# Optimization experiments

Measured on AMD Instinct MI355X. Metric: run time of the kernel, lower is better.

## Reference

```python
import jax, jax.numpy as jnp
import numpy as np

# dims
M, C, D = 64, 2000, 512          # clients, classes, embed_dim
H = 4                             # num_heads
HD = D // H                       # head_dim = 128
DFF = 2048                        # torch TransformerEncoderLayer default dim_feedforward
NUM_CLASSES = 2000
EPS = 1e-5


def _ln(x, g, b):
    mu = jnp.mean(x, axis=-1, keepdims=True)
    var = jnp.mean(jnp.square(x - mu), axis=-1, keepdims=True)
    return (x - mu) * jax.lax.rsqrt(var + EPS) * g + b


def setup_inputs() -> dict:
    key = jax.random.key(0)
    ks = jax.random.split(key, 16)
    s = 0.02
    return {
        "client_protos": jax.random.normal(ks[0], (M, C, D), jnp.float32),
        "norm_g": jnp.ones((D,), jnp.float32),
        "norm_b": jnp.zeros((D,), jnp.float32),
        "in_proj_w": jax.random.normal(ks[1], (3 * D, D), jnp.float32) * s,
        "in_proj_b": jnp.zeros((3 * D,), jnp.float32),
        "out_proj_w": jax.random.normal(ks[2], (D, D), jnp.float32) * s,
        "out_proj_b": jnp.zeros((D,), jnp.float32),
        "lin1_w": jax.random.normal(ks[3], (DFF, D), jnp.float32) * s,
        "lin1_b": jnp.zeros((DFF,), jnp.float32),
        "lin2_w": jax.random.normal(ks[4], (D, DFF), jnp.float32) * s,
        "lin2_b": jnp.zeros((D,), jnp.float32),
        "norm1_g": jnp.ones((D,), jnp.float32),
        "norm1_b": jnp.zeros((D,), jnp.float32),
        "norm2_g": jnp.ones((D,), jnp.float32),
        "norm2_b": jnp.zeros((D,), jnp.float32),
        "global_query": jax.random.normal(ks[5], (NUM_CLASSES, D), jnp.float32),
        "all_labels": jax.random.randint(ks[6], (C,), 0, NUM_CLASSES, jnp.int32),
        "round_num": 10,
        "client_idx": 0,
    }


def reference(client_protos, norm_g, norm_b, in_proj_w, in_proj_b,
              out_proj_w, out_proj_b, lin1_w, lin1_b, lin2_w, lin2_b,
              norm1_g, norm1_b, norm2_g, norm2_b, global_query,
              all_labels, round_num, client_idx):
    # 1) LayerNorm over all prototypes: (M, C, D)
    x = _ln(client_protos, norm_g, norm_b)
    # 2) Per-class transformer: original loops c in range(C) on (1, M, D).
    #    Batched: treat C as batch -> (C, M, D). Post-norm torch encoder layer.
    x = jnp.transpose(x, (1, 0, 2))  # (C, M, D)
    # self-attention
    qkv = x @ in_proj_w.T + in_proj_b          # (C, M, 3D)
    q, k, v = jnp.split(qkv, 3, axis=-1)
    q = q.reshape(C, M, H, HD)
    k = k.reshape(C, M, H, HD)
    v = v.reshape(C, M, H, HD)
    scores = jnp.einsum('cqhd,ckhd->chqk', q, k) / np.sqrt(HD).astype(np.float32)
    attn = jax.nn.softmax(scores, axis=-1)
    sa = jnp.einsum('chqk,ckhd->cqhd', attn, v).reshape(C, M, D)
    sa = sa @ out_proj_w.T + out_proj_b
    x = _ln(x + sa, norm1_g, norm1_b)
    # feed-forward (relu, dropout = eval no-op)
    ff = jax.nn.relu(x @ lin1_w.T + lin1_b) @ lin2_w.T + lin2_b
    x = _ln(x + ff, norm2_g, norm2_b)           # (C, M, D) == protos_trans^T
    # 3) Cross-attention with per-class global query
    q_all = global_query[all_labels].reshape(C, H, HD)
    kv_all = x.reshape(C, M, H, HD)
    s2 = jnp.einsum('chd,cmhd->chm', q_all, kv_all) / np.sqrt(HD).astype(np.float32)
    w2 = jax.nn.softmax(s2, axis=-1)
    attn_out = jnp.einsum('chm,cmhd->chd', w2, kv_all).reshape(C, D)
    return attn_out
```

## Files before the change

### kernel.cpp

```cpp
#include <hip/hip_runtime.h>

typedef _Float16 f16;
typedef _Float16 half4 __attribute__((ext_vector_type(4)));
typedef _Float16 half8 __attribute__((ext_vector_type(8)));
typedef float f32x4 __attribute__((ext_vector_type(4)));

typedef __attribute__((address_space(1))) void* as1v;
typedef __attribute__((address_space(3))) void* as3v;

#define SCALE 0.08838834764831845f

static __device__ __forceinline__ f32x4 mfma16(half8 a, half8 b, f32x4 c){
  return __builtin_amdgcn_mfma_f32_16x16x32_f16(a, b, c, 0, 0, 0);
}

__global__ __launch_bounds__(256) void k_cvt(const float* __restrict__ src, f16* __restrict__ dst, int n){
  int i = (blockIdx.x * 256 + threadIdx.x) * 8;
  if (i >= n) return;
  float4 a = *(const float4*)(src + i);
  float4 b = *(const float4*)(src + i + 4);
  half8 h;
  h[0] = (f16)a.x; h[1] = (f16)a.y; h[2] = (f16)a.z; h[3] = (f16)a.w;
  h[4] = (f16)b.x; h[5] = (f16)b.y; h[6] = (f16)b.z; h[7] = (f16)b.w;
  *(half8*)(dst + i) = h;
}

__global__ __launch_bounds__(256) void k_ln0(const float* __restrict__ protos,
                                             const float* __restrict__ g,
                                             const float* __restrict__ bb,
                                             f16* __restrict__ xb, int c0){
  const int w = threadIdx.x >> 6, l = threadIdx.x & 63;
  const int q = blockIdx.x * 4 + w;
  const int cl = q >> 6, m = q & 63;
  const float* in = protos + ((size_t)m * 2000 + (size_t)(c0 + cl)) * 512;
  const int d0 = l * 8;
  float4 a = *(const float4*)(in + d0);
  float4 c = *(const float4*)(in + d0 + 4);
  float s  = a.x + a.y + a.z + a.w + c.x + c.y + c.z + c.w;
  float ss = a.x*a.x + a.y*a.y + a.z*a.z + a.w*a.w + c.x*c.x + c.y*c.y + c.z*c.z + c.w*c.w;
#pragma unroll
  for (int msk = 1; msk < 64; msk <<= 1){ s += __shfl_xor(s, msk); ss += __shfl_xor(ss, msk); }
  const float mu = s * (1.f/512.f);
  const float rs = rsqrtf(ss * (1.f/512.f) - mu*mu + 1e-5f);
  float4 g0 = *(const float4*)(g + d0),  g1 = *(const float4*)(g + d0 + 4);
  float4 b0 = *(const float4*)(bb + d0), b1 = *(const float4*)(bb + d0 + 4);
  half8 o;
  o[0] = (f16)((a.x - mu) * rs * g0.x + b0.x);
  o[1] = (f16)((a.y - mu) * rs * g0.y + b0.y);
  o[2] = (f16)((a.z - mu) * rs * g0.z + b0.z);
  o[3] = (f16)((a.w - mu) * rs * g0.w + b0.w);
  o[4] = (f16)((c.x - mu) * rs * g1.x + b1.x);
  o[5] = (f16)((c.y - mu) * rs * g1.y + b1.y);
  o[6] = (f16)((c.z - mu) * rs * g1.z + b1.z);
  o[7] = (f16)((c.w - mu) * rs * g1.w + b1.w);
  *(half8*)(xb + (size_t)q * 512 + d0) = o;
}

__global__ __launch_bounds__(256) void k_resln(const f16* __restrict__ t, const f16* __restrict__ skip,
                                               const float* __restrict__ g, const float* __restrict__ bb,
                                               f16* __restrict__ outp){
  const int w = threadIdx.x >> 6, l = threadIdx.x & 63;
  const size_t q = (size_t)blockIdx.x * 4 + w;
  const int d0 = l * 8;
  half8 tv = *(const half8*)(t + q * 512 + d0);
  half8 sk = *(const half8*)(skip + q * 512 + d0);
  float v0 = (float)tv[0] + (float)sk[0], v1 = (float)tv[1] + (float)sk[1];
  float v2 = (float)tv[2] + (float)sk[2], v3 = (float)tv[3] + (float)sk[3];
  float v4 = (float)tv[4] + (float)sk[4], v5 = (float)tv[5] + (float)sk[5];
  float v6 = (float)tv[6] + (float)sk[6], v7 = (float)tv[7] + (float)sk[7];
  float s  = v0+v1+v2+v3+v4+v5+v6+v7;
  float ss = v0*v0+v1*v1+v2*v2+v3*v3+v4*v4+v5*v5+v6*v6+v7*v7;
#pragma unroll
  for (int msk = 1; msk < 64; msk <<= 1){ s += __shfl_xor(s, msk); ss += __shfl_xor(ss, msk); }
  const float mu = s * (1.f/512.f);
  const float rs = rsqrtf(ss * (1.f/512.f) - mu*mu + 1e-5f);
  float4 g0 = *(const float4*)(g + d0),  g1 = *(const float4*)(g + d0 + 4);
  float4 b0 = *(const float4*)(bb + d0), b1 = *(const float4*)(bb + d0 + 4);
  half8 o;
  o[0] = (f16)((v0 - mu) * rs * g0.x + b0.x);
  o[1] = (f16)((v1 - mu) * rs * g0.y + b0.y);
  o[2] = (f16)((v2 - mu) * rs * g0.z + b0.z);
  o[3] = (f16)((v3 - mu) * rs * g0.w + b0.w);
  o[4] = (f16)((v4 - mu) * rs * g1.x + b1.x);
  o[5] = (f16)((v5 - mu) * rs * g1.y + b1.y);
  o[6] = (f16)((v6 - mu) * rs * g1.z + b1.z);
  o[7] = (f16)((v7 - mu) * rs * g1.w + b1.w);
  *(half8*)(outp + q * 512 + d0) = o;
}

#define GLL(gp, lp) __builtin_amdgcn_global_load_lds((as1v)(void*)(gp), (as3v)(lp), 16, 0, 0)

template<bool RELU>
__global__ __launch_bounds__(512, 2) void k_gemm(const f16* __restrict__ A, const f16* __restrict__ B,
                                                 const float* __restrict__ bias, f16* __restrict__ Cout,
                                                 int N, int K, int gn){
  extern __shared__ char smem_raw[];
  f16* lds = (f16*)smem_raw;

  const int t = threadIdx.x, w = t >> 6, l = t & 63;
  const int wr = w >> 2, wc = w & 3;

  const int nwg = gridDim.x;
  const int q8 = nwg >> 3, r8 = nwg & 7;
  const int xcd = blockIdx.x & 7, lidx = blockIdx.x >> 3;
  const int swz = (xcd < r8 ? xcd * (q8 + 1) : r8 * (q8 + 1) + (xcd - r8) * q8) + lidx;
  const int tm = swz / gn, tn = swz % gn;
  const size_t row0 = (size_t)tm * 256;
  const int col0 = tn * 256;

  f32x4 acc[8][4];
#pragma unroll
  for (int m = 0; m < 8; ++m)
#pragma unroll
    for (int n = 0; n < 4; ++n) acc[m][n] = (f32x4){0.f,0.f,0.f,0.f};

  const int lsw = ((t & 7) ^ ((t >> 3) & 7)) * 8;
  const f16* gAb = A + (row0 + (size_t)(t >> 3)) * (size_t)K + lsw;
  const f16* gBb = B + ((size_t)col0 + (size_t)(t >> 3)) * (size_t)K + lsw;
  const int t8 = t * 8;

  const int rA  = (l & 15) * 64;
  const int ps0 = (((l >> 4) ^ (l & 7)) << 3);
  const int ps1 = (((4 + (l >> 4)) ^ (l & 7)) << 3);
  const int abase = wr * 8192 + rA;
  const int bbase = 16384 + wc * 4096 + rA;

  const int NT = K >> 6;

  auto stgA = [&](int tt, int h){
    f16* d = lds + (tt & 1) * 32768 + h * 8192 + t8;
    const f16* s = gAb + (size_t)(h * 128) * K + (size_t)tt * 64;
    GLL(s, d);
    GLL(s + (size_t)64 * K, d + 4096);
  };
  auto stgB = [&](int tt, int h){
    f16* d = lds + (tt & 1) * 32768 + 16384 + h * 8192 + t8;
    const f16* s = gBb + (size_t)(h * 128) * K + (size_t)tt * 64;
    GLL(s, d);
    GLL(s + (size_t)64 * K, d + 4096);
  };

  stgA(0, 0); stgA(0, 1); stgB(0, 0); stgB(0, 1);
  if (NT > 1){
    stgA(1, 0);
    asm volatile("s_waitcnt vmcnt(2)" ::: "memory");
  } else {
    asm volatile("s_waitcnt vmcnt(0)" ::: "memory");
  }
  __builtin_amdgcn_s_barrier();

  for (int tt = 0; tt < NT; ++tt){
    const f16* sb = lds + (tt & 1) * 32768;
    const bool s1 = tt + 1 < NT, s2 = tt + 2 < NT;
    half8 af03[4][2], af47[4][2], bf[4][2];

#pragma unroll
    for (int m = 0; m < 4; ++m){
      af03[m][0] = *(const half8*)(sb + abase + m * 1024 + ps0);
      af03[m][1] = *(const half8*)(sb + abase + m * 1024 + ps1);
    }
#pragma unroll
    for (int n = 0; n < 2; ++n){
      bf[n][0] = *(const half8*)(sb + bbase + n * 1024 + ps0);
      bf[n][1] = *(const half8*)(sb + bbase + n * 1024 + ps1);
    }
    if (s1) stgA(tt + 1, 1);
    __builtin_amdgcn_s_barrier();
    asm volatile("s_waitcnt lgkmcnt(0)" ::: "memory");
    __builtin_amdgcn_sched_barrier(0);
    __builtin_amdgcn_s_setprio(1);
#pragma unroll
    for (int ks = 0; ks < 2; ++ks)
#pragma unroll
      for (int m = 0; m < 4; ++m)
#pragma unroll
        for (int n = 0; n < 2; ++n)
          acc[m][n] = mfma16(bf[n][ks], af03[m][ks], acc[m][n]);
    __builtin_amdgcn_s_setprio(0);
    __builtin_amdgcn_s_barrier();

#pragma unroll
    for (int n = 2; n < 4; ++n){
      bf[n][0] = *(const half8*)(sb + bbase + n * 1024 + ps0);
      bf[n][1] = *(const half8*)(sb + bbase + n * 1024 + ps1);
    }
    if (s1) stgB(tt + 1, 0);
    __builtin_amdgcn_s_barrier();
    asm volatile("s_waitcnt lgkmcnt(0)" ::: "memory");
    __builtin_amdgcn_sched_barrier(0);
    __builtin_amdgcn_s_setprio(1);
#pragma unroll
    for (int ks = 0; ks < 2; ++ks)
#pragma unroll
      for (int m = 0; m < 4; ++m)
#pragma unroll
        for (int n = 2; n < 4; ++n)
          acc[m][n] = mfma16(bf[n][ks], af03[m][ks], acc[m][n]);
    __builtin_amdgcn_s_setprio(0);
    __builtin_amdgcn_s_barrier();

#pragma unroll
    for (int m = 0; m < 4; ++m){
      af47[m][0] = *(const half8*)(sb + abase + (m + 4) * 1024 + ps0);
      af47[m][1] = *(const half8*)(sb + abase + (m + 4) * 1024 + ps1);
    }
    if (s1) stgB(tt + 1, 1);
    __builtin_amdgcn_s_barrier();
    asm volatile("s_waitcnt lgkmcnt(0)" ::: "memory");
    __builtin_amdgcn_sched_barrier(0);
    __builtin_amdgcn_s_setprio(1);
#pragma unroll
    for (int ks = 0; ks < 2; ++ks)
#pragma unroll
      for (int m = 0; m < 4; ++m)
#pragma unroll
        for (int n = 0; n < 2; ++n)
          acc[m + 4][n] = mfma16(bf[n][ks], af47[m][ks], acc[m + 4][n]);
    __builtin_amdgcn_s_setprio(0);
    __builtin_amdgcn_s_barrier();

    if (s2) stgA(tt + 2, 0);
    __builtin_amdgcn_s_barrier();
    __builtin_amdgcn_s_setprio(1);
#pragma unroll
    for (int ks = 0; ks < 2; ++ks)
#pragma unroll
      for (int m = 0; m < 4; ++m)
#pragma unroll
        for (int n = 2; n < 4; ++n)
          acc[m + 4][n] = mfma16(bf[n][ks], af47[m][ks], acc[m + 4][n]);
    __builtin_amdgcn_s_setprio(0);
    if (s1){
      if (s2) { asm volatile("s_waitcnt vmcnt(2)" ::: "memory"); }
      else    { asm volatile("s_waitcnt vmcnt(0)" ::: "memory"); }
    }
    __builtin_amdgcn_s_barrier();
  }

#pragma unroll
  for (int n = 0; n < 4; ++n){
    const int c = col0 + wc * 64 + n * 16 + ((l >> 4) << 2);
    float4 b4 = *(const float4*)(bias + c);
#pragma unroll
    for (int m = 0; m < 8; ++m){
      const size_t r = row0 + (size_t)(wr * 128 + m * 16 + (l & 15));
      float v0 = acc[m][n][0] + b4.x;
      float v1 = acc[m][n][1] + b4.y;
      float v2 = acc[m][n][2] + b4.z;
      float v3 = acc[m][n][3] + b4.w;
      if (RELU){ v0 = fmaxf(v0, 0.f); v1 = fmaxf(v1, 0.f); v2 = fmaxf(v2, 0.f); v3 = fmaxf(v3, 0.f); }
      half4 h; h[0] = (f16)v0; h[1] = (f16)v1; h[2] = (f16)v2; h[3] = (f16)v3;
      *(half4*)&Cout[r * (size_t)N + c] = h;
    }
  }
}

__global__ __launch_bounds__(256) void k_attn(const f16* __restrict__ qkv, f16* __restrict__ sa){
  __shared__ __align__(16) f16 P[4][4096];
  __shared__ __align__(16) f16 VT[4][4096];
  const int cl = blockIdx.x;
  const int h = threadIdx.x >> 6, l = threadIdx.x & 63;
  const f16* base = qkv + (size_t)cl * 64 * 1536;
  const f16* Qp = base + h * 128;
  const f16* Kp = base + 512 + h * 128;
  const f16* Vp = base + 1024 + h * 128;

  f32x4 s[4][4];
#pragma unroll
  for (int x = 0; x < 4; ++x)
#pragma unroll
    for (int y = 0; y < 4; ++y) s[x][y] = (f32x4){0.f,0.f,0.f,0.f};
#pragma unroll
  for (int ks = 0; ks < 4; ++ks){
    half8 aq[4], bk[4];
#pragma unroll
    for (int x = 0; x < 4; ++x)
      aq[x] = *(const half8*)&Qp[(size_t)(x * 16 + (l & 15)) * 1536 + ks * 32 + (l >> 4) * 8];
#pragma unroll
    for (int y = 0; y < 4; ++y)
      bk[y] = *(const half8*)&Kp[(size_t)(y * 16 + (l & 15)) * 1536 + ks * 32 + (l >> 4) * 8];
#pragma unroll
    for (int x = 0; x < 4; ++x)
#pragma unroll
      for (int y = 0; y < 4; ++y)
        s[x][y] = mfma16(aq[x], bk[y], s[x][y]);
  }

  char* Pb = (char*)&P[h][0];
#pragma unroll
  for (int x = 0; x < 4; ++x){
#pragma unroll
    for (int j = 0; j < 4; ++j){
      float e0 = s[x][0][j] * SCALE;
      float e1 = s[x][1][j] * SCALE;
      float e2 = s[x][2][j] * SCALE;
      float e3 = s[x][3][j] * SCALE;
      float mx = fmaxf(fmaxf(e0, e1), fmaxf(e2, e3));
#pragma unroll
      for (int msk = 1; msk < 16; msk <<= 1) mx = fmaxf(mx, __shfl_xor(mx, msk));
      e0 = __expf(e0 - mx); e1 = __expf(e1 - mx); e2 = __expf(e2 - mx); e3 = __expf(e3 - mx);
      float sm = e0 + e1 + e2 + e3;
#pragma unroll
      for (int msk = 1; msk < 16; msk <<= 1) sm += __shfl_xor(sm, msk);
      const float inv = 1.f / sm;
      const int row = x * 16 + (l >> 4) * 4 + j;
      const int rb = row * 128 + (l & 15) * 2;
      const int rsw = (row & 7) << 4;
      *(f16*)(Pb + ((rb     ) ^ rsw)) = (f16)(e0 * inv);
      *(f16*)(Pb + ((rb + 32) ^ rsw)) = (f16)(e1 * inv);
      *(f16*)(Pb + ((rb + 64) ^ rsw)) = (f16)(e2 * inv);
      *(f16*)(Pb + ((rb + 96) ^ rsw)) = (f16)(e3 * inv);
    }
  }

  char* Vb = (char*)&VT[h][0];
#pragma unroll
  for (int dh = 0; dh < 2; ++dh){
#pragma unroll
    for (int it = 0; it < 8; ++it){
      const int chunk = it * 64 + l;
      const int m = chunk >> 3, dc = chunk & 7;
      half8 v = *(const half8*)&Vp[(size_t)m * 1536 + dh * 64 + dc * 8];
#pragma unroll
      for (int jj = 0; jj < 8; ++jj){
        const int dd = dc * 8 + jj;
        *(f16*)(Vb + ((dd * 128 + m * 2) ^ ((dd & 7) << 4))) = v[jj];
      }
    }
    __syncthreads();
#pragma unroll
    for (int x = 0; x < 4; ++x){
      const int ar = x * 16 + (l & 15);
      const int ab = ar * 128, sw = (ar & 7) << 4;
      half8 ap0 = *(const half8*)(Pb + ((ab + (l >> 4) * 16) ^ sw));
      half8 ap1 = *(const half8*)(Pb + ((ab + 64 + (l >> 4) * 16) ^ sw));
#pragma unroll
      for (int dt = 0; dt < 4; ++dt){
        const int vr = dt * 16 + (l & 15);
        const int vb = vr * 128, vsw = (vr & 7) << 4;
        half8 b0 = *(const half8*)(Vb + ((vb + (l >> 4) * 16) ^ vsw));
        half8 b1 = *(const half8*)(Vb + ((vb + 64 + (l >> 4) * 16) ^ vsw));
        f32x4 o = (f32x4){0.f,0.f,0.f,0.f};
        o = mfma16(ap0, b0, o);
        o = mfma16(ap1, b1, o);
#pragma unroll
        for (int j = 0; j < 4; ++j){
          const int mrow = x * 16 + (l >> 4) * 4 + j;
          const int dcol = dh * 64 + dt * 16 + (l & 15);
          sa[((size_t)cl * 64 + mrow) * 512 + h * 128 + dcol] = (f16)o[j];
        }
      }
    }
    __syncthreads();
  }
}

__global__ __launch_bounds__(256) void k_cross(const f16* __restrict__ z, const float* __restrict__ gq,
                                               const int* __restrict__ labels, float* __restrict__ out,
                                               int c0){
  const int cl = blockIdx.x;
  const int h = threadIdx.x >> 6, l = threadIdx.x & 63;
  const int cg = c0 + cl;
  const float* q = gq + (size_t)labels[cg] * 512 + h * 128;
  const f16* zb = z + (size_t)cl * 64 * 512 + h * 128;

  const f16* zr = zb + (size_t)l * 512;
  float s = 0.f;
#pragma unroll
  for (int d = 0; d < 128; d += 8){
    half8 v = *(const half8*)&zr[d];
    float4 q0 = *(const float4*)&q[d];
    float4 q1 = *(const float4*)&q[d + 4];
    s += q0.x*(float)v[0] + q0.y*(float)v[1] + q0.z*(float)v[2] + q0.w*(float)v[3]
       + q1.x*(float)v[4] + q1.y*(float)v[5] + q1.z*(float)v[6] + q1.w*(float)v[7];
  }
  s *= SCALE;
  float mx = s;
#pragma unroll
  for (int msk = 1; msk < 64; msk <<= 1) mx = fmaxf(mx, __shfl_xor(mx, msk));
  float e = __expf(s - mx);
  float sm = e;
#pragma unroll
  for (int msk = 1; msk < 64; msk <<= 1) sm += __shfl_xor(sm, msk);
  const float wgt = e / sm;

  float a0 = 0.f, a1 = 0.f;
  for (int m = 0; m < 64; ++m){
    const float wm = __shfl(wgt, m);
    const f16* zm = zb + (size_t)m * 512 + 2 * l;
    a0 += wm * (float)zm[0];
    a1 += wm * (float)zm[1];
  }
  float2 o; o.x = a0; o.y = a1;
  *(float2*)&out[(size_t)cg * 512 + h * 128 + 2 * l] = o;
}

extern "C" void kernel_launch(void* const* d_in, const int* in_sizes, int n_in,
                              void* d_out, int out_size, void* d_ws, size_t ws_size,
                              hipStream_t stream){
  (void)in_sizes; (void)n_in; (void)out_size;
  const float* protos = (const float*)d_in[0];
  const float* norm_g = (const float*)d_in[1];
  const float* norm_b = (const float*)d_in[2];
  const float* in_w   = (const float*)d_in[3];
  const float* in_b   = (const float*)d_in[4];
  const float* ow     = (const float*)d_in[5];
  const float* ob     = (const float*)d_in[6];
  const float* l1w    = (const float*)d_in[7];
  const float* l1b    = (const float*)d_in[8];
  const float* l2w    = (const float*)d_in[9];
  const float* l2b    = (const float*)d_in[10];
  const float* n1g    = (const float*)d_in[11];
  const float* n1b    = (const float*)d_in[12];
  const float* n2g    = (const float*)d_in[13];
  const float* n2b    = (const float*)d_in[14];
  const float* gq     = (const float*)d_in[15];
  const int*   labels = (const int*)d_in[16];
  float* out = (float*)d_out;

  char* p = (char*)d_ws;
  auto alloc = [&](size_t bytes)->char*{
    char* r = p; p += (bytes + 255) & ~(size_t)255; return r;
  };
  f16* Wq = (f16*)alloc((size_t)1536*512*2);
  f16* Wo = (f16*)alloc((size_t)512*512*2);
  f16* W1 = (f16*)alloc((size_t)2048*512*2);
  f16* W2 = (f16*)alloc((size_t)512*2048*2);
  const size_t fixed = (size_t)(p - (char*)d_ws);

  const size_t per_class = (size_t)64*512*2 + (size_t)64*2048*2 + (size_t)64*512*2 + (size_t)64*512*2;
  long long avail = (long long)ws_size - (long long)fixed - 8192;
  long long cc_max = avail > 0 ? avail / (long long)per_class : 0;
  int Cc = (int)(cc_max > 2000 ? 2000 : cc_max);
  Cc &= ~3;
  if (Cc < 4) Cc = 4;

  f16* xb  = (f16*)alloc((size_t)Cc*64*512*2);
  f16* big = (f16*)alloc((size_t)Cc*64*2048*2);
  f16* sac = (f16*)alloc((size_t)Cc*64*512*2);
  f16* tmp = (f16*)alloc((size_t)Cc*64*512*2);

  k_cvt<<<1536*512/2048, 256, 0, stream>>>(in_w, Wq, 1536*512);
  k_cvt<<<512*512/2048,  256, 0, stream>>>(ow,   Wo, 512*512);
  k_cvt<<<2048*512/2048, 256, 0, stream>>>(l1w,  W1, 2048*512);
  k_cvt<<<2048*512/2048, 256, 0, stream>>>(l2w,  W2, 512*2048);

  const size_t SMEM = 131072;
  for (int c0 = 0; c0 < 2000; c0 += Cc){
    const int cc = (2000 - c0 < Cc) ? (2000 - c0) : Cc;
    const int R = cc * 64;
    const int gm = R / 256;
    k_ln0<<<R/4, 256, 0, stream>>>(protos, norm_g, norm_b, xb, c0);
    k_gemm<false><<<gm*6, 512, SMEM, stream>>>(xb, Wq, in_b, big, 1536, 512, 6);
    k_attn<<<cc, 256, 0, stream>>>(big, sac);
    k_gemm<false><<<gm*2, 512, SMEM, stream>>>(sac, Wo, ob, tmp, 512, 512, 2);
    k_resln<<<R/4, 256, 0, stream>>>(tmp, xb, n1g, n1b, sac);
    k_gemm<true><<<gm*8, 512, SMEM, stream>>>(sac, W1, l1b, big, 2048, 512, 8);
    k_gemm<false><<<gm*2, 512, SMEM, stream>>>(big, W2, l2b, tmp, 512, 2048, 2);
    k_resln<<<R/4, 256, 0, stream>>>(tmp, sac, n2g, n2b, big);
    k_cross<<<cc, 256, 0, stream>>>(big, gq, labels, out, c0);
  }
}
```

Baseline: 1.497 ms.

## Fuse output-projection and FFN2 GEMMs with residual add and LayerNorm

```diff
diff --git a/kernel.cpp b/kernel.cpp
--- a/kernel.cpp
+++ b/kernel.cpp
@@ -56,38 +56,6 @@
   *(half8*)(xb + (size_t)q * 512 + d0) = o;
 }
 
-__global__ __launch_bounds__(256) void k_resln(const f16* __restrict__ t, const f16* __restrict__ skip,
-                                               const float* __restrict__ g, const float* __restrict__ bb,
-                                               f16* __restrict__ outp){
-  const int w = threadIdx.x >> 6, l = threadIdx.x & 63;
-  const size_t q = (size_t)blockIdx.x * 4 + w;
-  const int d0 = l * 8;
-  half8 tv = *(const half8*)(t + q * 512 + d0);
-  half8 sk = *(const half8*)(skip + q * 512 + d0);
-  float v0 = (float)tv[0] + (float)sk[0], v1 = (float)tv[1] + (float)sk[1];
-  float v2 = (float)tv[2] + (float)sk[2], v3 = (float)tv[3] + (float)sk[3];
-  float v4 = (float)tv[4] + (float)sk[4], v5 = (float)tv[5] + (float)sk[5];
-  float v6 = (float)tv[6] + (float)sk[6], v7 = (float)tv[7] + (float)sk[7];
-  float s  = v0+v1+v2+v3+v4+v5+v6+v7;
-  float ss = v0*v0+v1*v1+v2*v2+v3*v3+v4*v4+v5*v5+v6*v6+v7*v7;
-#pragma unroll
-  for (int msk = 1; msk < 64; msk <<= 1){ s += __shfl_xor(s, msk); ss += __shfl_xor(ss, msk); }
-  const float mu = s * (1.f/512.f);
-  const float rs = rsqrtf(ss * (1.f/512.f) - mu*mu + 1e-5f);
-  float4 g0 = *(const float4*)(g + d0),  g1 = *(const float4*)(g + d0 + 4);
-  float4 b0 = *(const float4*)(bb + d0), b1 = *(const float4*)(bb + d0 + 4);
-  half8 o;
-  o[0] = (f16)((v0 - mu) * rs * g0.x + b0.x);
-  o[1] = (f16)((v1 - mu) * rs * g0.y + b0.y);
-  o[2] = (f16)((v2 - mu) * rs * g0.z + b0.z);
-  o[3] = (f16)((v3 - mu) * rs * g0.w + b0.w);
-  o[4] = (f16)((v4 - mu) * rs * g1.x + b1.x);
-  o[5] = (f16)((v5 - mu) * rs * g1.y + b1.y);
-  o[6] = (f16)((v6 - mu) * rs * g1.z + b1.z);
-  o[7] = (f16)((v7 - mu) * rs * g1.w + b1.w);
-  *(half8*)(outp + q * 512 + d0) = o;
-}
-
 #define GLL(gp, lp) __builtin_amdgcn_global_load_lds((as1v)(void*)(gp), (as3v)(lp), 16, 0, 0)
 
 template<bool RELU>
@@ -251,6 +219,121 @@
       if (RELU){ v0 = fmaxf(v0, 0.f); v1 = fmaxf(v1, 0.f); v2 = fmaxf(v2, 0.f); v3 = fmaxf(v3, 0.f); }
       half4 h; h[0] = (f16)v0; h[1] = (f16)v1; h[2] = (f16)v2; h[3] = (f16)v3;
       *(half4*)&Cout[r * (size_t)N + c] = h;
+    }
+  }
+}
+
+__global__ __launch_bounds__(512, 2) void k_gemm_ln(const f16* __restrict__ A, const f16* __restrict__ B,
+                                                    const float* __restrict__ bias,
+                                                    const f16* __restrict__ skip,
+                                                    const float* __restrict__ gam,
+                                                    const float* __restrict__ bet,
+                                                    f16* __restrict__ Cout, int K){
+  extern __shared__ char smem_raw[];
+  f16* lds = (f16*)smem_raw;
+
+  const int t = threadIdx.x, w = t >> 6, l = t & 63;
+  const int wr = w >> 2, wc = w & 3;
+
+  const int nwg = gridDim.x;
+  const int q8 = nwg >> 3, r8 = nwg & 7;
+  const int xcd = blockIdx.x & 7, lidx = blockIdx.x >> 3;
+  const int tm = (xcd < r8 ? xcd * (q8 + 1) : r8 * (q8 + 1) + (xcd - r8) * q8) + lidx;
+  const size_t row0 = (size_t)tm * 128;
+
+  f32x4 acc[4][8];
+#pragma unroll
+  for (int m = 0; m < 4; ++m)
+#pragma unroll
+    for (int n = 0; n < 8; ++n) acc[m][n] = (f32x4){0.f,0.f,0.f,0.f};
+
+  const int ssl = ((t & 3) ^ ((t >> 3) & 3)) * 8;
+  const f16* gA = A + (row0 + (size_t)(t >> 2)) * (size_t)K + ssl;
+  const f16* gB = B + (size_t)(t >> 2) * (size_t)K + ssl;
+  const int t8 = t * 8;
+
+  const int psl = (((l >> 4) ^ ((l >> 1) & 3)) << 3);
+  const int abase = (wr * 64 + (l & 15)) * 32 + psl;
+  const int bbase = 4096 + (wc * 128 + (l & 15)) * 32 + psl;
+
+  const int NT = K >> 5;
+
+  auto stage = [&](int tt){
+    f16* buf = lds + (tt & 1) * 20480;
+    const size_t ko = (size_t)tt * 32;
+    GLL(gA + ko, buf + t8);
+#pragma unroll
+    for (int i = 0; i < 4; ++i)
+      GLL(gB + ko + (size_t)(i * 128) * K, buf + 4096 + i * 4096 + t8);
+  };
+
+  stage(0);
+  __syncthreads();
+
+  for (int tk = 0; tk < NT; ++tk){
+    if (tk + 1 < NT) stage(tk + 1);
+    const f16* sb = lds + (tk & 1) * 20480;
+    half8 af[4], bf[8];
+#pragma unroll
+    for (int m = 0; m < 4; ++m) af[m] = *(const half8*)(sb + abase + m * 512);
+#pragma unroll
+    for (int n = 0; n < 8; ++n) bf[n] = *(const half8*)(sb + bbase + n * 512);
+#pragma unroll
+    for (int m = 0; m < 4; ++m)
+#pragma unroll
+      for (int n = 0; n < 8; ++n)
+        acc[m][n] = mfma16(bf[n], af[m], acc[m][n]);
+    __syncthreads();
+  }
+
+  float2* part = (float2*)lds;
+
+#pragma unroll
+  for (int m = 0; m < 4; ++m){
+    const size_t r = row0 + (size_t)(wr * 64 + m * 16 + (l & 15));
+    float s = 0.f, ss = 0.f;
+#pragma unroll
+    for (int n = 0; n < 8; ++n){
+      const int c = wc * 128 + n * 16 + ((l >> 4) << 2);
+      float4 b4 = *(const float4*)(bias + c);
+      half4 sk = *(const half4*)(skip + r * 512 + c);
+      float v0 = acc[m][n][0] + b4.x + (float)sk[0];
+      float v1 = acc[m][n][1] + b4.y + (float)sk[1];
+      float v2 = acc[m][n][2] + b4.z + (float)sk[2];
+      float v3 = acc[m][n][3] + b4.w + (float)sk[3];
+      acc[m][n][0] = v0; acc[m][n][1] = v1; acc[m][n][2] = v2; acc[m][n][3] = v3;
+      s  += v0 + v1 + v2 + v3;
+      ss += v0*v0 + v1*v1 + v2*v2 + v3*v3;
+    }
+    s += __shfl_xor(s, 16); ss += __shfl_xor(ss, 16);
+    s += __shfl_xor(s, 32); ss += __shfl_xor(ss, 32);
+    if ((l >> 4) == 0){
+      float2 p; p.x = s; p.y = ss;
+      part[wc * 128 + wr * 64 + m * 16 + l] = p;
+    }
+  }
+  __syncthreads();
+
+#pragma unroll
+  for (int m = 0; m < 4; ++m){
+    const int rl = wr * 64 + m * 16 + (l & 15);
+    const size_t r = row0 + (size_t)rl;
+    float2 p0 = part[rl], p1 = part[128 + rl], p2 = part[256 + rl], p3 = part[384 + rl];
+    const float s  = p0.x + p1.x + p2.x + p3.x;
+    const float ss = p0.y + p1.y + p2.y + p3.y;
+    const float mu = s * (1.f/512.f);
+    const float rs = rsqrtf(ss * (1.f/512.f) - mu*mu + 1e-5f);
+#pragma unroll
+    for (int n = 0; n < 8; ++n){
+      const int c = wc * 128 + n * 16 + ((l >> 4) << 2);
+      float4 g4 = *(const float4*)(gam + c);
+      float4 b4 = *(const float4*)(bet + c);
+      half4 h;
+      h[0] = (f16)((acc[m][n][0] - mu) * rs * g4.x + b4.x);
+      h[1] = (f16)((acc[m][n][1] - mu) * rs * g4.y + b4.y);
+      h[2] = (f16)((acc[m][n][2] - mu) * rs * g4.z + b4.z);
+      h[3] = (f16)((acc[m][n][3] - mu) * rs * g4.w + b4.w);
+      *(half4*)&Cout[r * 512 + c] = h;
     }
   }
 }
@@ -445,7 +528,8 @@
   k_cvt<<<2048*512/2048, 256, 0, stream>>>(l1w,  W1, 2048*512);
   k_cvt<<<2048*512/2048, 256, 0, stream>>>(l2w,  W2, 512*2048);
 
-  const size_t SMEM = 131072;
+  const size_t SMEM  = 131072;
+  const size_t SMEML = 81920;
   for (int c0 = 0; c0 < 2000; c0 += Cc){
     const int cc = (2000 - c0 < Cc) ? (2000 - c0) : Cc;
     const int R = cc * 64;
@@ -453,11 +537,9 @@
     k_ln0<<<R/4, 256, 0, stream>>>(protos, norm_g, norm_b, xb, c0);
     k_gemm<false><<<gm*6, 512, SMEM, stream>>>(xb, Wq, in_b, big, 1536, 512, 6);
     k_attn<<<cc, 256, 0, stream>>>(big, sac);
-    k_gemm<false><<<gm*2, 512, SMEM, stream>>>(sac, Wo, ob, tmp, 512, 512, 2);
-    k_resln<<<R/4, 256, 0, stream>>>(tmp, xb, n1g, n1b, sac);
-    k_gemm<true><<<gm*8, 512, SMEM, stream>>>(sac, W1, l1b, big, 2048, 512, 8);
-    k_gemm<false><<<gm*2, 512, SMEM, stream>>>(big, W2, l2b, tmp, 512, 2048, 2);
-    k_resln<<<R/4, 256, 0, stream>>>(tmp, sac, n2g, n2b, big);
-    k_cross<<<cc, 256, 0, stream>>>(big, gq, labels, out, c0);
-  }
-}
+    k_gemm_ln<<<R/128, 512, SMEML, stream>>>(sac, Wo, ob, xb, n1g, n1b, tmp, 512);
+    k_gemm<true><<<gm*8, 512, SMEM, stream>>>(tmp, W1, l1b, big, 2048, 512, 8);
+    k_gemm_ln<<<R/128, 512, SMEML, stream>>>(big, W2, l2b, tmp, n2g, n2b, sac, 2048);
+    k_cross<<<cc, 256, 0, stream>>>(sac, gq, labels, out, c0);
+  }
+}
```

Result: slower. 1.570 ms (+4.9%).

## Make GEMMs persistent over tile ranges and fuse final LayerNorm into cross-attention

Applied to the files above, without the earlier changes.

```diff
diff --git a/kernel.cpp b/kernel.cpp
--- a/kernel.cpp
+++ b/kernel.cpp
@@ -93,20 +93,24 @@
 template<bool RELU>
 __global__ __launch_bounds__(512, 2) void k_gemm(const f16* __restrict__ A, const f16* __restrict__ B,
                                                  const float* __restrict__ bias, f16* __restrict__ Cout,
-                                                 int N, int K, int gn){
+                                                 int N, int K, int gm, int gn){
   extern __shared__ char smem_raw[];
   f16* lds = (f16*)smem_raw;
 
   const int t = threadIdx.x, w = t >> 6, l = t & 63;
   const int wr = w >> 2, wc = w & 3;
 
-  const int nwg = gridDim.x;
-  const int q8 = nwg >> 3, r8 = nwg & 7;
-  const int xcd = blockIdx.x & 7, lidx = blockIdx.x >> 3;
-  const int swz = (xcd < r8 ? xcd * (q8 + 1) : r8 * (q8 + 1) + (xcd - r8) * q8) + lidx;
-  const int tm = swz / gn, tn = swz % gn;
-  const size_t row0 = (size_t)tm * 256;
-  const int col0 = tn * 256;
+  const int ntiles = gm * gn;
+  const int nb = gridDim.x;
+  const int chunk = ntiles / nb, rem = ntiles - chunk * nb;
+  const int b = blockIdx.x;
+  const int i0 = b * chunk + (b < rem ? b : rem);
+  const int cnt = chunk + (b < rem ? 1 : 0);
+  if (cnt == 0) return;
+
+  const int NT = K >> 6;
+  const int lnt = __ffs(NT) - 1;
+  const int G = cnt * NT;
 
   f32x4 acc[8][4];
 #pragma unroll
@@ -115,8 +119,8 @@
     for (int n = 0; n < 4; ++n) acc[m][n] = (f32x4){0.f,0.f,0.f,0.f};
 
   const int lsw = ((t & 7) ^ ((t >> 3) & 7)) * 8;
-  const f16* gAb = A + (row0 + (size_t)(t >> 3)) * (size_t)K + lsw;
-  const f16* gBb = B + ((size_t)col0 + (size_t)(t >> 3)) * (size_t)K + lsw;
+  const f16* gAt = A + (size_t)(t >> 3) * (size_t)K + lsw;
+  const f16* gBt = B + (size_t)(t >> 3) * (size_t)K + lsw;
   const int t8 = t * 8;
 
   const int rA  = (l & 15) * 64;
@@ -125,23 +129,29 @@
   const int abase = wr * 8192 + rA;
   const int bbase = 16384 + wc * 4096 + rA;
 
-  const int NT = K >> 6;
-
-  auto stgA = [&](int tt, int h){
-    f16* d = lds + (tt & 1) * 32768 + h * 8192 + t8;
-    const f16* s = gAb + (size_t)(h * 128) * K + (size_t)tt * 64;
+  auto stgA = [&](int g, int h){
+    if (g >= G) return;
+    const int idx = i0 + (g >> lnt);
+    const int kt  = g & (NT - 1);
+    const int tm  = idx % gm;
+    f16* d = lds + (g & 1) * 32768 + h * 8192 + t8;
+    const f16* s = gAt + ((size_t)(tm * 256 + h * 128)) * (size_t)K + (size_t)kt * 64;
     GLL(s, d);
     GLL(s + (size_t)64 * K, d + 4096);
   };
-  auto stgB = [&](int tt, int h){
-    f16* d = lds + (tt & 1) * 32768 + 16384 + h * 8192 + t8;
-    const f16* s = gBb + (size_t)(h * 128) * K + (size_t)tt * 64;
+  auto stgB = [&](int g, int h){
+    if (g >= G) return;
+    const int idx = i0 + (g >> lnt);
+    const int kt  = g & (NT - 1);
+    const int tn  = idx / gm;
+    f16* d = lds + (g & 1) * 32768 + 16384 + h * 8192 + t8;
+    const f16* s = gBt + ((size_t)(tn * 256 + h * 128)) * (size_t)K + (size_t)kt * 64;
     GLL(s, d);
     GLL(s + (size_t)64 * K, d + 4096);
   };
 
   stgA(0, 0); stgA(0, 1); stgB(0, 0); stgB(0, 1);
-  if (NT > 1){
+  if (G > 1){
     stgA(1, 0);
     asm volatile("s_waitcnt vmcnt(2)" ::: "memory");
   } else {
@@ -149,9 +159,9 @@
   }
   __builtin_amdgcn_s_barrier();
 
-  for (int tt = 0; tt < NT; ++tt){
-    const f16* sb = lds + (tt & 1) * 32768;
-    const bool s1 = tt + 1 < NT, s2 = tt + 2 < NT;
+  for (int g = 0; g < G; ++g){
+    const f16* sb = lds + (g & 1) * 32768;
+    const bool s1 = g + 1 < G, s2 = g + 2 < G;
     half8 af03[4][2], af47[4][2], bf[4][2];
 
 #pragma unroll
@@ -164,7 +174,7 @@
       bf[n][0] = *(const half8*)(sb + bbase + n * 1024 + ps0);
       bf[n][1] = *(const half8*)(sb + bbase + n * 1024 + ps1);
     }
-    if (s1) stgA(tt + 1, 1);
+    stgA(g + 1, 1);
     __builtin_amdgcn_s_barrier();
     asm volatile("s_waitcnt lgkmcnt(0)" ::: "memory");
     __builtin_amdgcn_sched_barrier(0);
@@ -184,7 +194,7 @@
       bf[n][0] = *(const half8*)(sb + bbase + n * 1024 + ps0);
       bf[n][1] = *(const half8*)(sb + bbase + n * 1024 + ps1);
     }
-    if (s1) stgB(tt + 1, 0);
+    stgB(g + 1, 0);
     __builtin_amdgcn_s_barrier();
     asm volatile("s_waitcnt lgkmcnt(0)" ::: "memory");
     __builtin_amdgcn_sched_barrier(0);
@@ -204,7 +214,7 @@
       af47[m][0] = *(const half8*)(sb + abase + (m + 4) * 1024 + ps0);
       af47[m][1] = *(const half8*)(sb + abase + (m + 4) * 1024 + ps1);
     }
-    if (s1) stgB(tt + 1, 1);
+    stgB(g + 1, 1);
     __builtin_amdgcn_s_barrier();
     asm volatile("s_waitcnt lgkmcnt(0)" ::: "memory");
     __builtin_amdgcn_sched_barrier(0);
@@ -219,7 +229,7 @@
     __builtin_amdgcn_s_setprio(0);
     __builtin_amdgcn_s_barrier();
 
-    if (s2) stgA(tt + 2, 0);
+    stgA(g + 2, 0);
     __builtin_amdgcn_s_barrier();
     __builtin_amdgcn_s_setprio(1);
 #pragma unroll
@@ -235,22 +245,29 @@
       else    { asm volatile("s_waitcnt vmcnt(0)" ::: "memory"); }
     }
     __builtin_amdgcn_s_barrier();
-  }
-
-#pragma unroll
-  for (int n = 0; n < 4; ++n){
-    const int c = col0 + wc * 64 + n * 16 + ((l >> 4) << 2);
-    float4 b4 = *(const float4*)(bias + c);
-#pragma unroll
-    for (int m = 0; m < 8; ++m){
-      const size_t r = row0 + (size_t)(wr * 128 + m * 16 + (l & 15));
-      float v0 = acc[m][n][0] + b4.x;
-      float v1 = acc[m][n][1] + b4.y;
-      float v2 = acc[m][n][2] + b4.z;
-      float v3 = acc[m][n][3] + b4.w;
-      if (RELU){ v0 = fmaxf(v0, 0.f); v1 = fmaxf(v1, 0.f); v2 = fmaxf(v2, 0.f); v3 = fmaxf(v3, 0.f); }
-      half4 h; h[0] = (f16)v0; h[1] = (f16)v1; h[2] = (f16)v2; h[3] = (f16)v3;
-      *(half4*)&Cout[r * (size_t)N + c] = h;
+
+    if ((g & (NT - 1)) == NT - 1){
+      const int idx = i0 + (g >> lnt);
+      const int tm = idx % gm, tn = idx / gm;
+      const size_t row0 = (size_t)tm * 256;
+      const int col0 = tn * 256;
+#pragma unroll
+      for (int n = 0; n < 4; ++n){
+        const int c = col0 + wc * 64 + n * 16 + ((l >> 4) << 2);
+        float4 b4 = *(const float4*)(bias + c);
+#pragma unroll
+        for (int m = 0; m < 8; ++m){
+          const size_t r = row0 + (size_t)(wr * 128 + m * 16 + (l & 15));
+          float v0 = acc[m][n][0] + b4.x;
+          float v1 = acc[m][n][1] + b4.y;
+          float v2 = acc[m][n][2] + b4.z;
+          float v3 = acc[m][n][3] + b4.w;
+          if (RELU){ v0 = fmaxf(v0, 0.f); v1 = fmaxf(v1, 0.f); v2 = fmaxf(v2, 0.f); v3 = fmaxf(v3, 0.f); }
+          half4 h; h[0] = (f16)v0; h[1] = (f16)v1; h[2] = (f16)v2; h[3] = (f16)v3;
+          *(half4*)&Cout[r * (size_t)N + c] = h;
+          acc[m][n] = (f32x4){0.f,0.f,0.f,0.f};
+        }
+      }
     }
   }
 }
@@ -355,20 +372,56 @@
   }
 }
 
-__global__ __launch_bounds__(256) void k_cross(const f16* __restrict__ z, const float* __restrict__ gq,
-                                               const int* __restrict__ labels, float* __restrict__ out,
-                                               int c0){
+#define ZOFF(m, cb) (((m) * 1024 + (cb)) ^ (((m) & 7) << 4))
+__global__ __launch_bounds__(256) void k_resln_cross(const f16* __restrict__ t, const f16* __restrict__ skip,
+                                                     const float* __restrict__ g, const float* __restrict__ bb,
+                                                     const float* __restrict__ gq, const int* __restrict__ labels,
+                                                     float* __restrict__ out, int c0){
+  __shared__ __align__(16) char Z[65536];
   const int cl = blockIdx.x;
-  const int h = threadIdx.x >> 6, l = threadIdx.x & 63;
+  const int w = threadIdx.x >> 6, l = threadIdx.x & 63;
   const int cg = c0 + cl;
+  const size_t rbase = (size_t)cl * 64 * 512;
+  const int d0 = l * 8;
+
+  float4 g0 = *(const float4*)(g + d0),  g1 = *(const float4*)(g + d0 + 4);
+  float4 b0 = *(const float4*)(bb + d0), b1 = *(const float4*)(bb + d0 + 4);
+
+#pragma unroll 4
+  for (int i = 0; i < 16; ++i){
+    const int m = w * 16 + i;
+    const size_t q = rbase + (size_t)m * 512;
+    half8 tv = *(const half8*)(t + q + d0);
+    half8 sk = *(const half8*)(skip + q + d0);
+    float v0 = (float)tv[0] + (float)sk[0], v1 = (float)tv[1] + (float)sk[1];
+    float v2 = (float)tv[2] + (float)sk[2], v3 = (float)tv[3] + (float)sk[3];
+    float v4 = (float)tv[4] + (float)sk[4], v5 = (float)tv[5] + (float)sk[5];
+    float v6 = (float)tv[6] + (float)sk[6], v7 = (float)tv[7] + (float)sk[7];
+    float s  = v0+v1+v2+v3+v4+v5+v6+v7;
+    float ss = v0*v0+v1*v1+v2*v2+v3*v3+v4*v4+v5*v5+v6*v6+v7*v7;
+#pragma unroll
+    for (int msk = 1; msk < 64; msk <<= 1){ s += __shfl_xor(s, msk); ss += __shfl_xor(ss, msk); }
+    const float mu = s * (1.f/512.f);
+    const float rs = rsqrtf(ss * (1.f/512.f) - mu*mu + 1e-5f);
+    half8 o;
+    o[0] = (f16)((v0 - mu) * rs * g0.x + b0.x);
+    o[1] = (f16)((v1 - mu) * rs * g0.y + b0.y);
+    o[2] = (f16)((v2 - mu) * rs * g0.z + b0.z);
+    o[3] = (f16)((v3 - mu) * rs * g0.w + b0.w);
+    o[4] = (f16)((v4 - mu) * rs * g1.x + b1.x);
+    o[5] = (f16)((v5 - mu) * rs * g1.y + b1.y);
+    o[6] = (f16)((v6 - mu) * rs * g1.z + b1.z);
+    o[7] = (f16)((v7 - mu) * rs * g1.w + b1.w);
+    *(half8*)(Z + ZOFF(m, l * 16)) = o;
+  }
+  __syncthreads();
+
+  const int h = w;
   const float* q = gq + (size_t)labels[cg] * 512 + h * 128;
-  const f16* zb = z + (size_t)cl * 64 * 512 + h * 128;
-
-  const f16* zr = zb + (size_t)l * 512;
   float s = 0.f;
 #pragma unroll
   for (int d = 0; d < 128; d += 8){
-    half8 v = *(const half8*)&zr[d];
+    half8 v = *(const half8*)(Z + ZOFF(l, (h * 128 + d) * 2));
     float4 q0 = *(const float4*)&q[d];
     float4 q1 = *(const float4*)&q[d + 4];
     s += q0.x*(float)v[0] + q0.y*(float)v[1] + q0.z*(float)v[2] + q0.w*(float)v[3]
@@ -387,7 +440,7 @@
   float a0 = 0.f, a1 = 0.f;
   for (int m = 0; m < 64; ++m){
     const float wm = __shfl(wgt, m);
-    const f16* zm = zb + (size_t)m * 512 + 2 * l;
+    const f16* zm = (const f16*)(Z + ZOFF(m, (h * 128 + 2 * l) * 2));
     a0 += wm * (float)zm[0];
     a1 += wm * (float)zm[1];
   }
@@ -451,13 +504,12 @@
     const int R = cc * 64;
     const int gm = R / 256;
     k_ln0<<<R/4, 256, 0, stream>>>(protos, norm_g, norm_b, xb, c0);
-    k_gemm<false><<<gm*6, 512, SMEM, stream>>>(xb, Wq, in_b, big, 1536, 512, 6);
+    k_gemm<false><<<512, 512, SMEM, stream>>>(xb, Wq, in_b, big, 1536, 512, gm, 6);
     k_attn<<<cc, 256, 0, stream>>>(big, sac);
-    k_gemm<false><<<gm*2, 512, SMEM, stream>>>(sac, Wo, ob, tmp, 512, 512, 2);
+    k_gemm<false><<<512, 512, SMEM, stream>>>(sac, Wo, ob, tmp, 512, 512, gm, 2);
     k_resln<<<R/4, 256, 0, stream>>>(tmp, xb, n1g, n1b, sac);
-    k_gemm<true><<<gm*8, 512, SMEM, stream>>>(sac, W1, l1b, big, 2048, 512, 8);
-    k_gemm<false><<<gm*2, 512, SMEM, stream>>>(big, W2, l2b, tmp, 512, 2048, 2);
-    k_resln<<<R/4, 256, 0, stream>>>(tmp, sac, n2g, n2b, big);
-    k_cross<<<cc, 256, 0, stream>>>(big, gq, labels, out, c0);
-  }
-}
+    k_gemm<true><<<512, 512, SMEM, stream>>>(sac, W1, l1b, big, 2048, 512, gm, 8);
+    k_gemm<false><<<512, 512, SMEM, stream>>>(big, W2, l2b, tmp, 512, 2048, gm, 2);
+    k_resln_cross<<<cc, 256, 0, stream>>>(tmp, sac, n2g, n2b, gq, labels, out, c0);
+  }
+}
```

Result: slower. 1.602 ms (+7.1%).
